# Optimization experiments

Measured on AMD Instinct MI355X. Metric: run time of the kernel, lower is better.

Reference implementation:

```python
import jax, jax.numpy as jnp
import numpy as np

B, S, H, NH, D = 8, 512, 1024, 16, 64
SCALE = float(np.sqrt(D))

def _linear_params(key, name, d_in, d_out):
    k1, k2 = jax.random.split(key)
    lim = 1.0 / np.sqrt(d_in)
    W = jax.random.uniform(k1, (d_out, d_in), jnp.float32, -lim, lim)
    b = jax.random.uniform(k2, (d_out,), jnp.float32, -lim, lim)
    return W, b

def setup_inputs() -> dict:
    key = jax.random.key(0)
    ks = jax.random.split(key, 16)
    inp = {
        'query_states': jax.random.normal(ks[0], (B, S, H), jnp.float32),
        'key_states': jax.random.normal(ks[1], (B, S, H), jnp.float32),
        'value_states': jax.random.normal(ks[2], (B, S, H), jnp.float32),
        'attention_mask': jnp.zeros((B, 1, S, S), jnp.float32),
        'position_embedding': jax.random.normal(ks[3], (B, S, H), jnp.float32),
        'feat_embedding': jax.random.normal(ks[4], (B, S, H), jnp.float32),
    }
    names = ['q', 'k', 'v', 'qp', 'kp', 'qf', 'kf', 'd']
    for i, n in enumerate(names):
        W, b = _linear_params(ks[5 + i], n, H, H)
        inp['W' + n] = W
        inp['b' + n] = b
    return inp

def _heads(x):
    # [B,S,H] -> [B,NH,S,D]
    return x.reshape(B, S, NH, D).transpose(0, 2, 1, 3)

def _lin(x, W, b):
    return jnp.einsum('bsh,oh->bso', x, W) + b

def reference(query_states, key_states, value_states, attention_mask,
              position_embedding, feat_embedding,
              Wq, bq, Wk, bk, Wv, bv, Wqp, bqp, Wkp, bkp,
              Wqf, bqf, Wkf, bkf, Wd, bd):
    q = _heads(_lin(query_states, Wq, bq))
    k = _heads(_lin(key_states, Wk, bk))
    v = _heads(_lin(value_states, Wv, bv))
    qp = _heads(_lin(position_embedding, Wqp, bqp))
    kp = _heads(_lin(position_embedding, Wkp, bkp))
    qf = _heads(_lin(feat_embedding, Wqf, bqf))
    kf = _heads(_lin(feat_embedding, Wkf, bkf))

    attention_map = jnp.einsum('bhqd,bhkd->bhqk', q, k)        # content scores
    pos_map = jnp.einsum('bhqd,bhkd->bhqk', qp, kp)             # position scores
    feat_map = jnp.einsum('bhqd,bhkd->bhqk', qf, kf)            # feature scores

    scores = (attention_map + pos_map + feat_map) / SCALE + attention_mask
    probs = jax.nn.softmax(scores, axis=-1)
    ctx = jnp.einsum('bhqk,bhkd->bhqd', probs, v)
    ctx = ctx.transpose(0, 2, 1, 3).reshape(B, S, H)
    hidden_states = jnp.einsum('bsh,oh->bso', ctx, Wd) + bd
    return hidden_states, attention_map
```

## Files before the change

### kernel.cpp

```cpp
#include <hip/hip_runtime.h>

#define B_  8
#define S_  512
#define H_  1024
#define NH_ 16
#define D_  64
#define M_  4096
#define HH_ ((size_t)H_ * H_)
#define MH_ ((size_t)M_ * H_)

typedef __attribute__((ext_vector_type(8))) short short8;
typedef __attribute__((ext_vector_type(4))) float f32x4;

__device__ __forceinline__ unsigned short f2bf(float f) {
    unsigned u = __float_as_uint(f);
    return (unsigned short)((u + 0x7fffu + ((u >> 16) & 1u)) >> 16);
}
__device__ __forceinline__ void gload_lds16(const void* g, void* l) {
    __builtin_amdgcn_global_load_lds(
        (const __attribute__((address_space(1))) void*)g,
        (__attribute__((address_space(3))) void*)l, 16, 0, 0);
}

struct CvtArgs { const float* src[8]; unsigned short* dst[8]; };

__global__ __launch_bounds__(256) void cvt_kernel(CvtArgs a) {
    const int seg = blockIdx.y;
    const float* s = a.src[seg];
    unsigned short* d = a.dst[seg];
    const size_t i = ((size_t)blockIdx.x * 256 + threadIdx.x) * 4;
    float4 f = *(const float4*)(s + i);
    union { unsigned long long v; unsigned short h[4]; } pk;
    pk.h[0] = f2bf(f.x); pk.h[1] = f2bf(f.y);
    pk.h[2] = f2bf(f.z); pk.h[3] = f2bf(f.w);
    *(unsigned long long*)(d + i) = pk.v;
}

struct GemmPtrs { const void* x; const unsigned short* w; const float* bias; void* o; };
struct GemmArgs { GemmPtrs p[7]; };

template <bool A_FP32, bool OUT_BF16>
__global__ __launch_bounds__(256) void mfma_gemm(GemmArgs args) {
    const GemmPtrs gp = args.p[blockIdx.z];
    __shared__ unsigned short As[128 * 32];
    __shared__ unsigned short Bs[128 * 32];

    const int tid  = threadIdx.x;
    const int wave = tid >> 6, lane = tid & 63;
    const int row0 = blockIdx.y * 128, col0 = blockIdx.x * 128;
    const int wr = (wave & 1) * 64, wc = (wave >> 1) * 64;
    const int lr = lane & 15;

    const int br1 = tid >> 2,      bq1 = (tid & 3) ^ ((br1 >> 1) & 3);
    const int p2  = tid + 256;
    const int br2 = p2 >> 2,       bq2 = (p2 & 3) ^ ((br2 >> 1) & 3);

    const unsigned short* wp1 = gp.w + (size_t)(col0 + br1) * H_ + bq1 * 8;
    const unsigned short* wp2 = gp.w + (size_t)(col0 + br2) * H_ + bq2 * 8;
    unsigned short* bd1 = Bs + tid * 8;
    unsigned short* bd2 = Bs + (tid + 256) * 8;

    const unsigned short* ap1 =
        (const unsigned short*)gp.x + (size_t)(row0 + br1) * H_ + bq1 * 8;
    const unsigned short* ap2 =
        (const unsigned short*)gp.x + (size_t)(row0 + br2) * H_ + bq2 * 8;
    unsigned short* ad1 = As + tid * 8;
    unsigned short* ad2 = As + (tid + 256) * 8;

    const int ar = tid >> 1, ah = tid & 1, asw = (ar >> 1) & 3;
    const int g0 = (ah * 2) ^ asw, g1 = (ah * 2 + 1) ^ asw;
    const float* ax = (const float*)gp.x + (size_t)(row0 + ar) * H_ + ah * 16;

    const int slot8 = (((lane >> 4) ^ ((lr >> 1) & 3)) << 3);

    f32x4 acc[4][4];
#pragma unroll
    for (int mi = 0; mi < 4; ++mi)
#pragma unroll
        for (int ni = 0; ni < 4; ++ni) acc[mi][ni] = (f32x4)0.f;

    for (int k0 = 0; k0 < H_; k0 += 32) {
        __syncthreads();
        if (A_FP32) {
            float4 f0 = *(const float4*)(ax + k0);
            float4 f1 = *(const float4*)(ax + k0 + 4);
            float4 f2 = *(const float4*)(ax + k0 + 8);
            float4 f3 = *(const float4*)(ax + k0 + 12);
            union { short8 v; unsigned short h[8]; } u0, u1;
            u0.h[0] = f2bf(f0.x); u0.h[1] = f2bf(f0.y);
            u0.h[2] = f2bf(f0.z); u0.h[3] = f2bf(f0.w);
            u0.h[4] = f2bf(f1.x); u0.h[5] = f2bf(f1.y);
            u0.h[6] = f2bf(f1.z); u0.h[7] = f2bf(f1.w);
            u1.h[0] = f2bf(f2.x); u1.h[1] = f2bf(f2.y);
            u1.h[2] = f2bf(f2.z); u1.h[3] = f2bf(f2.w);
            u1.h[4] = f2bf(f3.x); u1.h[5] = f2bf(f3.y);
            u1.h[6] = f2bf(f3.z); u1.h[7] = f2bf(f3.w);
            *(short8*)(As + ar * 32 + g0 * 8) = u0.v;
            *(short8*)(As + ar * 32 + g1 * 8) = u1.v;
        } else {
            gload_lds16(ap1 + k0, ad1);
            gload_lds16(ap2 + k0, ad2);
        }
        gload_lds16(wp1 + k0, bd1);
        gload_lds16(wp2 + k0, bd2);
        __syncthreads();

        short8 af[4], bfr[4];
#pragma unroll
        for (int mi = 0; mi < 4; ++mi)
            af[mi] = *(const short8*)(As + (wr + mi * 16 + lr) * 32 + slot8);
#pragma unroll
        for (int ni = 0; ni < 4; ++ni)
            bfr[ni] = *(const short8*)(Bs + (wc + ni * 16 + lr) * 32 + slot8);
#pragma unroll
        for (int mi = 0; mi < 4; ++mi)
#pragma unroll
            for (int ni = 0; ni < 4; ++ni)
                acc[mi][ni] = __builtin_amdgcn_mfma_f32_16x16x32_bf16(
                    af[mi], bfr[ni], acc[mi][ni], 0, 0, 0);
    }

    float bv[4];
#pragma unroll
    for (int ni = 0; ni < 4; ++ni)
        bv[ni] = gp.bias[col0 + wc + ni * 16 + lr];

#pragma unroll
    for (int mi = 0; mi < 4; ++mi)
#pragma unroll
        for (int r = 0; r < 4; ++r) {
            const int row = row0 + wr + mi * 16 + (lane >> 4) * 4 + r;
#pragma unroll
            for (int ni = 0; ni < 4; ++ni) {
                const int col = col0 + wc + ni * 16 + lr;
                const float v = acc[mi][ni][r] + bv[ni];
                if (OUT_BF16)
                    ((unsigned short*)gp.o)[(size_t)row * H_ + col] = f2bf(v);
                else
                    ((float*)gp.o)[(size_t)row * H_ + col] = v;
            }
        }
}

__global__ __launch_bounds__(256) void attn_kernel(
        const unsigned short* __restrict__ ws,
        const float* __restrict__ mask,
        float* __restrict__ amap,
        unsigned short* __restrict__ ctxo) {
    const unsigned short* qm0 = ws;
    const unsigned short* qm1 = ws + 3 * MH_;
    const unsigned short* qm2 = ws + 5 * MH_;
    const unsigned short* km0 = ws + 1 * MH_;
    const unsigned short* km1 = ws + 4 * MH_;
    const unsigned short* km2 = ws + 6 * MH_;
    const unsigned short* vm  = ws + 2 * MH_;

    __shared__ unsigned short Ks[3][64 * 64];
    __shared__ unsigned short Vt[64 * 64];
    __shared__ unsigned short Ps[4][16 * 64];

    const int qt  = blockIdx.x;
    const int bh  = blockIdx.y;
    const int b   = bh >> 4, h = bh & 15;
    const int tid = threadIdx.x;
    const int w   = tid >> 6, lane = tid & 63;
    const int lr  = lane & 15, g = lane >> 4;

    short8 qc[2], qp_[2], qf_[2];
    {
        const int qrow = qt * 64 + w * 16 + lr;
        const size_t base = ((size_t)(b * S_) + qrow) * H_ + h * D_ + g * 8;
#pragma unroll
        for (int kc = 0; kc < 2; ++kc) {
            qc[kc]  = *(const short8*)(qm0 + base + kc * 32);
            qp_[kc] = *(const short8*)(qm1 + base + kc * 32);
            qf_[kc] = *(const short8*)(qm2 + base + kc * 32);
        }
    }

    const int p1 = tid,        r1 = p1 >> 3, s1 = (p1 & 7) ^ (r1 & 7);
    const int p2 = tid + 256,  r2 = p2 >> 3, s2 = (p2 & 7) ^ (r2 & 7);
    const size_t kb1 = ((size_t)(b * S_) + r1) * H_ + h * D_ + s1 * 8;
    const size_t kb2 = ((size_t)(b * S_) + r2) * H_ + h * D_ + s2 * 8;
    unsigned short* kd1[3] = { Ks[0] + p1 * 8, Ks[1] + p1 * 8, Ks[2] + p1 * 8 };
    unsigned short* kd2[3] = { Ks[0] + p2 * 8, Ks[1] + p2 * 8, Ks[2] + p2 * 8 };
    const unsigned short* ksrc[3] = { km0, km1, km2 };

    const int vk  = (tid & 31) * 2;
    const int vdg = tid >> 5;
    const unsigned short* vp0 = vm + ((size_t)(b * S_) + vk) * H_ + h * D_ + vdg * 8;

    const int soffA = ((0 + g) ^ (lr & 7)) * 8;
    const int soffB = ((4 + g) ^ (lr & 7)) * 8;

    f32x4 oacc[4];
    float mrun[4], lrun[4];
#pragma unroll
    for (int i = 0; i < 4; ++i) {
        oacc[i] = (f32x4)0.f; mrun[i] = -1e30f; lrun[i] = 0.f;
    }

    for (int t = 0; t < 8; ++t) {
        const size_t koff = (size_t)(t * 64) * H_;
        __syncthreads();

        union { uint4 u; unsigned short h[8]; } va, vb;
        va.u = *(const uint4*)(vp0 + koff);
        vb.u = *(const uint4*)(vp0 + koff + H_);

#pragma unroll
        for (int m = 0; m < 3; ++m) {
            gload_lds16(ksrc[m] + kb1 + koff, kd1[m]);
            gload_lds16(ksrc[m] + kb2 + koff, kd2[m]);
        }

#pragma unroll
        for (int j = 0; j < 8; ++j) {
            const int d = vdg * 8 + j;
            const unsigned pk = (unsigned)va.h[j] | ((unsigned)vb.h[j] << 16);
            *(unsigned*)(Vt + d * 64 + (((vk >> 3) ^ (d & 7)) * 8) + (vk & 7)) = pk;
        }
        __syncthreads();

        f32x4 accC[4], accS[4];
#pragma unroll
        for (int ni = 0; ni < 4; ++ni) { accC[ni] = (f32x4)0.f; accS[ni] = (f32x4)0.f; }
#pragma unroll
        for (int ni = 0; ni < 4; ++ni) {
            const int rowb = (ni * 16 + lr) * 64;
            short8 c0 = *(const short8*)(Ks[0] + rowb + soffA);
            short8 c1 = *(const short8*)(Ks[0] + rowb + soffB);
            short8 p0 = *(const short8*)(Ks[1] + rowb + soffA);
            short8 p1f = *(const short8*)(Ks[1] + rowb + soffB);
            short8 f0 = *(const short8*)(Ks[2] + rowb + soffA);
            short8 f1 = *(const short8*)(Ks[2] + rowb + soffB);
            accC[ni] = __builtin_amdgcn_mfma_f32_16x16x32_bf16(qc[0], c0, accC[ni], 0, 0, 0);
            accC[ni] = __builtin_amdgcn_mfma_f32_16x16x32_bf16(qc[1], c1, accC[ni], 0, 0, 0);
            accS[ni] = __builtin_amdgcn_mfma_f32_16x16x32_bf16(qp_[0], p0, accS[ni], 0, 0, 0);
            accS[ni] = __builtin_amdgcn_mfma_f32_16x16x32_bf16(qp_[1], p1f, accS[ni], 0, 0, 0);
            accS[ni] = __builtin_amdgcn_mfma_f32_16x16x32_bf16(qf_[0], f0, accS[ni], 0, 0, 0);
            accS[ni] = __builtin_amdgcn_mfma_f32_16x16x32_bf16(qf_[1], f1, accS[ni], 0, 0, 0);
        }

        const int key0 = t * 64;
        float st[4][4];
#pragma unroll
        for (int ni = 0; ni < 4; ++ni) {
            const int col = key0 + ni * 16 + lr;
#pragma unroll
            for (int r = 0; r < 4; ++r) {
                const int row = qt * 64 + w * 16 + g * 4 + r;
                amap[((size_t)bh * S_ + row) * S_ + col] = accC[ni][r];
                const float mval =
                    mask[(size_t)b * S_ * S_ + (size_t)row * S_ + col];
                st[ni][r] = (accC[ni][r] + accS[ni][r]) * 0.125f + mval;
            }
        }

#pragma unroll
        for (int r = 0; r < 4; ++r) {
            float tmax = fmaxf(fmaxf(st[0][r], st[1][r]),
                               fmaxf(st[2][r], st[3][r]));
#pragma unroll
            for (int off = 8; off >= 1; off >>= 1)
                tmax = fmaxf(tmax, __shfl_xor(tmax, off));
            const float mnew = fmaxf(mrun[r], tmax);
            const float e0 = __expf(st[0][r] - mnew);
            const float e1 = __expf(st[1][r] - mnew);
            const float e2 = __expf(st[2][r] - mnew);
            const float e3 = __expf(st[3][r] - mnew);
            float esum = (e0 + e1) + (e2 + e3);
#pragma unroll
            for (int off = 8; off >= 1; off >>= 1)
                esum += __shfl_xor(esum, off);
            const float alpha = __expf(mrun[r] - mnew);
            lrun[r] = lrun[r] * alpha + esum;
            mrun[r] = mnew;
#pragma unroll
            for (int nd = 0; nd < 4; ++nd) oacc[nd][r] *= alpha;

            const int prow = g * 4 + r;
            unsigned short* pb = Ps[w] + prow * 64;
            const int sw = prow & 7, lh = lr >> 3, lw = lr & 7;
            pb[((0 + lh) ^ sw) * 8 + lw] = f2bf(e0);
            pb[((2 + lh) ^ sw) * 8 + lw] = f2bf(e1);
            pb[((4 + lh) ^ sw) * 8 + lw] = f2bf(e2);
            pb[((6 + lh) ^ sw) * 8 + lw] = f2bf(e3);
        }

#pragma unroll
        for (int kc = 0; kc < 2; ++kc) {
            const int soff = kc ? soffB : soffA;
            short8 pa = *(const short8*)(Ps[w] + lr * 64 + soff);
#pragma unroll
            for (int nd = 0; nd < 4; ++nd) {
                short8 vb2 = *(const short8*)(Vt + (nd * 16 + lr) * 64 + soff);
                oacc[nd] = __builtin_amdgcn_mfma_f32_16x16x32_bf16(
                    pa, vb2, oacc[nd], 0, 0, 0);
            }
        }
    }

#pragma unroll
    for (int r = 0; r < 4; ++r) {
        const float inv = 1.0f / lrun[r];
        const int row = qt * 64 + w * 16 + g * 4 + r;
#pragma unroll
        for (int nd = 0; nd < 4; ++nd)
            ctxo[((size_t)(b * S_) + row) * H_ + h * D_ + nd * 16 + lr] =
                f2bf(oacc[nd][r] * inv);
    }
}

extern "C" void kernel_launch(void* const* d_in, const int* in_sizes, int n_in,
                              void* d_out, int out_size, void* d_ws, size_t ws_size,
                              hipStream_t stream) {
    const float* in[22];
    for (int i = 0; i < 22; ++i) in[i] = (const float*)d_in[i];

    unsigned short* wsW = (unsigned short*)d_ws;
    unsigned short* wsP = wsW + 8 * HH_;
    unsigned short* wsC = wsP + 7 * MH_;
    float*          out = (float*)d_out;

    CvtArgs ca;
    {
        const int widx[8] = { 6, 8, 10, 12, 14, 16, 18, 20 };
        for (int i = 0; i < 8; ++i) { ca.src[i] = in[widx[i]]; ca.dst[i] = wsW + i * HH_; }
    }
    cvt_kernel<<<dim3(1024, 8), 256, 0, stream>>>(ca);

    GemmArgs ga;
    ga.p[0] = { in[0], wsW + 0 * HH_, in[7],  wsP + 0 * MH_ };
    ga.p[1] = { in[1], wsW + 1 * HH_, in[9],  wsP + 1 * MH_ };
    ga.p[2] = { in[2], wsW + 2 * HH_, in[11], wsP + 2 * MH_ };
    ga.p[3] = { in[4], wsW + 3 * HH_, in[13], wsP + 3 * MH_ };
    ga.p[4] = { in[4], wsW + 4 * HH_, in[15], wsP + 4 * MH_ };
    ga.p[5] = { in[5], wsW + 5 * HH_, in[17], wsP + 5 * MH_ };
    ga.p[6] = { in[5], wsW + 6 * HH_, in[19], wsP + 6 * MH_ };
    mfma_gemm<true, true><<<dim3(8, 32, 7), 256, 0, stream>>>(ga);

    attn_kernel<<<dim3(S_ / 64, B_ * NH_), 256, 0, stream>>>(
        wsP, in[3], out + MH_, wsC);

    GemmArgs gf;
    gf.p[0] = { wsC, wsW + 7 * HH_, in[21], out };
    for (int i = 1; i < 7; ++i) gf.p[i] = gf.p[0];
    mfma_gemm<false, false><<<dim3(8, 32, 1), 256, 0, stream>>>(gf);
}
```

Measured before the change: 492.8 us.

## Pre-convert activations to bf16, double-buffer GEMM LDS, and remap blocks across XCDs

The conversion kernel now also turns the five fp32 activation inputs into bf16 workspace buffers, so the projection GEMM reads bf16 A tiles through direct global-to-LDS loads. Previously each K-step converted fp32 in registers. The GEMM now double-buffers the A and B LDS tiles, issuing the next tile's loads before computing on the current one, with one barrier per iteration. Both the GEMMs and the attention kernel use a flat 1D grid whose block index is permuted so that neighbouring tiles land on the same XCD, aiming at better L2 reuse. In exchange there is an extra full activation conversion pass, more workspace, and double the GEMM shared memory, which may reduce occupancy.

```diff
diff --git a/kernel.cpp b/kernel.cpp
--- a/kernel.cpp
+++ b/kernel.cpp
@@ -22,7 +22,7 @@
         (__attribute__((address_space(3))) void*)l, 16, 0, 0);
 }
 
-struct CvtArgs { const float* src[8]; unsigned short* dst[8]; };
+struct CvtArgs { const float* src[28]; unsigned short* dst[28]; };
 
 __global__ __launch_bounds__(256) void cvt_kernel(CvtArgs a) {
     const int seg = blockIdx.y;
@@ -36,18 +36,26 @@
     *(unsigned long long*)(d + i) = pk.v;
 }
 
-struct GemmPtrs { const void* x; const unsigned short* w; const float* bias; void* o; };
+struct GemmPtrs { const unsigned short* x; const unsigned short* w;
+                  const float* bias; void* o; };
 struct GemmArgs { GemmPtrs p[7]; };
 
-template <bool A_FP32, bool OUT_BF16>
-__global__ __launch_bounds__(256) void mfma_gemm(GemmArgs args) {
-    const GemmPtrs gp = args.p[blockIdx.z];
-    __shared__ unsigned short As[128 * 32];
-    __shared__ unsigned short Bs[128 * 32];
+template <bool OUT_BF16>
+__global__ __launch_bounds__(256) void mfma_gemm(GemmArgs args, int nwg) {
+    const int dd  = blockIdx.x;
+    const int cpx = nwg >> 3;
+    const int l   = (dd & 7) * cpx + (dd >> 3);
+    const int bz  = l >> 8;
+    const int rem = l & 255;
+    const int by  = rem >> 3, bx = rem & 7;
+    const GemmPtrs gp = args.p[bz];
+
+    __shared__ unsigned short As[2][128 * 32];
+    __shared__ unsigned short Bs[2][128 * 32];
 
     const int tid  = threadIdx.x;
     const int wave = tid >> 6, lane = tid & 63;
-    const int row0 = blockIdx.y * 128, col0 = blockIdx.x * 128;
+    const int row0 = by * 128, col0 = bx * 128;
     const int wr = (wave & 1) * 64, wc = (wave >> 1) * 64;
     const int lr = lane & 15;
 
@@ -55,21 +63,10 @@
     const int p2  = tid + 256;
     const int br2 = p2 >> 2,       bq2 = (p2 & 3) ^ ((br2 >> 1) & 3);
 
+    const unsigned short* ap1 = gp.x + (size_t)(row0 + br1) * H_ + bq1 * 8;
+    const unsigned short* ap2 = gp.x + (size_t)(row0 + br2) * H_ + bq2 * 8;
     const unsigned short* wp1 = gp.w + (size_t)(col0 + br1) * H_ + bq1 * 8;
     const unsigned short* wp2 = gp.w + (size_t)(col0 + br2) * H_ + bq2 * 8;
-    unsigned short* bd1 = Bs + tid * 8;
-    unsigned short* bd2 = Bs + (tid + 256) * 8;
-
-    const unsigned short* ap1 =
-        (const unsigned short*)gp.x + (size_t)(row0 + br1) * H_ + bq1 * 8;
-    const unsigned short* ap2 =
-        (const unsigned short*)gp.x + (size_t)(row0 + br2) * H_ + bq2 * 8;
-    unsigned short* ad1 = As + tid * 8;
-    unsigned short* ad2 = As + (tid + 256) * 8;
-
-    const int ar = tid >> 1, ah = tid & 1, asw = (ar >> 1) & 3;
-    const int g0 = (ah * 2) ^ asw, g1 = (ah * 2 + 1) ^ asw;
-    const float* ax = (const float*)gp.x + (size_t)(row0 + ar) * H_ + ah * 16;
 
     const int slot8 = (((lane >> 4) ^ ((lr >> 1) & 3)) << 3);
 
@@ -79,45 +76,40 @@
 #pragma unroll
         for (int ni = 0; ni < 4; ++ni) acc[mi][ni] = (f32x4)0.f;
 
-    for (int k0 = 0; k0 < H_; k0 += 32) {
-        __syncthreads();
-        if (A_FP32) {
-            float4 f0 = *(const float4*)(ax + k0);
-            float4 f1 = *(const float4*)(ax + k0 + 4);
-            float4 f2 = *(const float4*)(ax + k0 + 8);
-            float4 f3 = *(const float4*)(ax + k0 + 12);
-            union { short8 v; unsigned short h[8]; } u0, u1;
-            u0.h[0] = f2bf(f0.x); u0.h[1] = f2bf(f0.y);
-            u0.h[2] = f2bf(f0.z); u0.h[3] = f2bf(f0.w);
-            u0.h[4] = f2bf(f1.x); u0.h[5] = f2bf(f1.y);
-            u0.h[6] = f2bf(f1.z); u0.h[7] = f2bf(f1.w);
-            u1.h[0] = f2bf(f2.x); u1.h[1] = f2bf(f2.y);
-            u1.h[2] = f2bf(f2.z); u1.h[3] = f2bf(f2.w);
-            u1.h[4] = f2bf(f3.x); u1.h[5] = f2bf(f3.y);
-            u1.h[6] = f2bf(f3.z); u1.h[7] = f2bf(f3.w);
-            *(short8*)(As + ar * 32 + g0 * 8) = u0.v;
-            *(short8*)(As + ar * 32 + g1 * 8) = u1.v;
-        } else {
-            gload_lds16(ap1 + k0, ad1);
-            gload_lds16(ap2 + k0, ad2);
-        }
-        gload_lds16(wp1 + k0, bd1);
-        gload_lds16(wp2 + k0, bd2);
-        __syncthreads();
-
+    gload_lds16(ap1, As[0] + tid * 8);
+    gload_lds16(ap2, As[0] + (tid + 256) * 8);
+    gload_lds16(wp1, Bs[0] + tid * 8);
+    gload_lds16(wp2, Bs[0] + (tid + 256) * 8);
+    __syncthreads();
+
+    int cur = 0;
+    for (int t = 0; t < 32; ++t) {
+        if (t < 31) {
+            const int k1 = (t + 1) * 32;
+            gload_lds16(ap1 + k1, As[cur ^ 1] + tid * 8);
+            gload_lds16(ap2 + k1, As[cur ^ 1] + (tid + 256) * 8);
+            gload_lds16(wp1 + k1, Bs[cur ^ 1] + tid * 8);
+            gload_lds16(wp2 + k1, Bs[cur ^ 1] + (tid + 256) * 8);
+        }
+
+        const unsigned short* Ab = As[cur];
+        const unsigned short* Bb = Bs[cur];
         short8 af[4], bfr[4];
 #pragma unroll
         for (int mi = 0; mi < 4; ++mi)
-            af[mi] = *(const short8*)(As + (wr + mi * 16 + lr) * 32 + slot8);
+            af[mi] = *(const short8*)(Ab + (wr + mi * 16 + lr) * 32 + slot8);
 #pragma unroll
         for (int ni = 0; ni < 4; ++ni)
-            bfr[ni] = *(const short8*)(Bs + (wc + ni * 16 + lr) * 32 + slot8);
+            bfr[ni] = *(const short8*)(Bb + (wc + ni * 16 + lr) * 32 + slot8);
 #pragma unroll
         for (int mi = 0; mi < 4; ++mi)
 #pragma unroll
             for (int ni = 0; ni < 4; ++ni)
                 acc[mi][ni] = __builtin_amdgcn_mfma_f32_16x16x32_bf16(
                     af[mi], bfr[ni], acc[mi][ni], 0, 0, 0);
+
+        __syncthreads();
+        cur ^= 1;
     }
 
     float bv[4];
@@ -159,8 +151,10 @@
     __shared__ unsigned short Vt[64 * 64];
     __shared__ unsigned short Ps[4][16 * 64];
 
-    const int qt  = blockIdx.x;
-    const int bh  = blockIdx.y;
+    const int blk = blockIdx.x;
+    const int l   = (blk & 7) * 128 + (blk >> 3);
+    const int qt  = l & 7;
+    const int bh  = l >> 3;
     const int b   = bh >> 4, h = bh & 15;
     const int tid = threadIdx.x;
     const int w   = tid >> 6, lane = tid & 63;
@@ -321,30 +315,40 @@
     unsigned short* wsW = (unsigned short*)d_ws;
     unsigned short* wsP = wsW + 8 * HH_;
     unsigned short* wsC = wsP + 7 * MH_;
+    unsigned short* wsA = wsC + 1 * MH_;
     float*          out = (float*)d_out;
 
     CvtArgs ca;
     {
+        int ci = 0;
         const int widx[8] = { 6, 8, 10, 12, 14, 16, 18, 20 };
-        for (int i = 0; i < 8; ++i) { ca.src[i] = in[widx[i]]; ca.dst[i] = wsW + i * HH_; }
-    }
-    cvt_kernel<<<dim3(1024, 8), 256, 0, stream>>>(ca);
+        for (int i = 0; i < 8; ++i, ++ci) {
+            ca.src[ci] = in[widx[i]];
+            ca.dst[ci] = wsW + i * HH_;
+        }
+        const int aidx[5] = { 0, 1, 2, 4, 5 };
+        for (int i = 0; i < 5; ++i)
+            for (int c = 0; c < 4; ++c, ++ci) {
+                ca.src[ci] = in[aidx[i]] + (size_t)c * HH_;
+                ca.dst[ci] = wsA + i * MH_ + (size_t)c * HH_;
+            }
+    }
+    cvt_kernel<<<dim3(1024, 28), 256, 0, stream>>>(ca);
 
     GemmArgs ga;
-    ga.p[0] = { in[0], wsW + 0 * HH_, in[7],  wsP + 0 * MH_ };
-    ga.p[1] = { in[1], wsW + 1 * HH_, in[9],  wsP + 1 * MH_ };
-    ga.p[2] = { in[2], wsW + 2 * HH_, in[11], wsP + 2 * MH_ };
-    ga.p[3] = { in[4], wsW + 3 * HH_, in[13], wsP + 3 * MH_ };
-    ga.p[4] = { in[4], wsW + 4 * HH_, in[15], wsP + 4 * MH_ };
-    ga.p[5] = { in[5], wsW + 5 * HH_, in[17], wsP + 5 * MH_ };
-    ga.p[6] = { in[5], wsW + 6 * HH_, in[19], wsP + 6 * MH_ };
-    mfma_gemm<true, true><<<dim3(8, 32, 7), 256, 0, stream>>>(ga);
-
-    attn_kernel<<<dim3(S_ / 64, B_ * NH_), 256, 0, stream>>>(
-        wsP, in[3], out + MH_, wsC);
+    ga.p[0] = { wsA + 0 * MH_, wsW + 0 * HH_, in[7],  wsP + 0 * MH_ };
+    ga.p[1] = { wsA + 1 * MH_, wsW + 1 * HH_, in[9],  wsP + 1 * MH_ };
+    ga.p[2] = { wsA + 2 * MH_, wsW + 2 * HH_, in[11], wsP + 2 * MH_ };
+    ga.p[3] = { wsA + 3 * MH_, wsW + 3 * HH_, in[13], wsP + 3 * MH_ };
+    ga.p[4] = { wsA + 3 * MH_, wsW + 4 * HH_, in[15], wsP + 4 * MH_ };
+    ga.p[5] = { wsA + 4 * MH_, wsW + 5 * HH_, in[17], wsP + 5 * MH_ };
+    ga.p[6] = { wsA + 4 * MH_, wsW + 6 * HH_, in[19], wsP + 6 * MH_ };
+    mfma_gemm<true><<<dim3(1792), 256, 0, stream>>>(ga, 1792);
+
+    attn_kernel<<<dim3(1024), 256, 0, stream>>>(wsP, in[3], out + MH_, wsC);
 
     GemmArgs gf;
     gf.p[0] = { wsC, wsW + 7 * HH_, in[21], out };
     for (int i = 1; i < 7; ++i) gf.p[i] = gf.p[0];
-    mfma_gemm<false, false><<<dim3(8, 32, 1), 256, 0, stream>>>(gf);
-}
+    mfma_gemm<false><<<dim3(256), 256, 0, stream>>>(gf, 256);
+}
```

Measured after the change: 428.4 us. -13.1%, faster.
